# Kernel optimization log

Hardware: AMD Instinct MI355X
Metric: run time of the kernel (lower is better)

Reference implementation:

```python
import math
import jax, jax.numpy as jnp
import numpy as np

NQ = 4   # n_qubits
NL = 2   # n_layers
H = 16   # num_heads


def _apply_gate(state, gate, q, batched):
    """Apply a 1-qubit gate on wire q to batched state [N, 2**NQ]."""
    n = state.shape[0]
    left, right = 2 ** q, 2 ** (NQ - 1 - q)
    s = state.reshape(n, left, 2, right)
    eq = 'nab,nlbr->nlar' if batched else 'ab,nlbr->nlar'
    return jnp.einsum(eq, gate, s).reshape(n, 2 ** NQ)


def _rot(phi, theta, omega):
    """PennyLane Rot(phi, theta, omega) = RZ(omega) RY(theta) RZ(phi), 2x2 unitary."""
    c = jnp.cos(theta / 2).astype(jnp.complex64)
    s = jnp.sin(theta / 2).astype(jnp.complex64)
    ep = jnp.exp(-0.5j * (phi + omega).astype(jnp.complex64))
    em = jnp.exp(0.5j * (phi - omega).astype(jnp.complex64))
    m00 = ep * c
    m01 = -em * s
    m10 = jnp.conj(em) * s
    m11 = jnp.conj(ep) * c
    return jnp.stack([jnp.stack([m00, m01]), jnp.stack([m10, m11])])


def _cnot01(state):
    """CNOT with control wire 0, target wire 1 on [N, 16]."""
    n = state.shape[0]
    s = state.reshape(n, 2, 2, 2 ** (NQ - 2))
    s = jnp.stack([s[:, 0], s[:, 1, ::-1]], axis=1)
    return s.reshape(n, 2 ** NQ)


def _quantum_block(inputs, params):
    """Analytic state-vector simulation of the PennyLane circuit.

    inputs: [N, NQ] rotation angles (AngleEmbedding, default RX).
    params: [NL, NQ, 3] Rot parameters.
    Returns [N, NQ] Pauli-Z expectation values.
    """
    n = inputs.shape[0]
    state = jnp.zeros((n, 2 ** NQ), jnp.complex64).at[:, 0].set(1.0)
    # AngleEmbedding: RX(inputs[:, q]) on wire q
    for q in range(NQ):
        a = inputs[:, q] * 0.5
        c = jnp.cos(a).astype(jnp.complex64)
        s = (-1j) * jnp.sin(a).astype(jnp.complex64)
        gate = jnp.stack([jnp.stack([c, s], -1), jnp.stack([s, c], -1)], -2)  # [N,2,2]
        state = _apply_gate(state, gate, q, batched=True)
    # Variational layers
    for l in range(NL):
        for q in range(NQ):
            g = _rot(params[l, q, 0], params[l, q, 1], params[l, q, 2])
            state = _apply_gate(state, g, q, batched=False)
        state = _cnot01(state)
    probs = (jnp.abs(state) ** 2).reshape(n, 2, 2, 2, 2)
    z = jnp.array([1.0, -1.0], probs.dtype)
    letters = 'abcd'
    evs = [jnp.einsum(f'nabcd,{letters[i]}->n', probs, z) for i in range(NQ)]
    return jnp.stack(evs, axis=-1)


def reference(x, params, w_q, w_k, w_v, w_o):
    B, S, E = x.shape
    dk = E // H

    def proj(w):
        return (x @ w.T).reshape(B, S, H, dk).transpose(0, 2, 1, 3)  # [B,H,S,dk]

    q, k, v = proj(w_q), proj(w_k), proj(w_v)

    def inject(t):
        ang = t[..., :NQ].reshape(-1, NQ)
        ev = _quantum_block(ang, params).reshape(B, H, S, NQ).astype(t.dtype)
        return t.at[..., :NQ].set(ev)

    q, k, v = inject(q), inject(k), inject(v)
    scores = jnp.einsum('bhqd,bhkd->bhqk', q, k) / math.sqrt(dk)
    attn = jax.nn.softmax(scores, axis=-1)
    out = jnp.einsum('bhqk,bhkd->bhqd', attn, v)
    out = out.transpose(0, 2, 1, 3).reshape(B, S, E)
    return out @ w_o.T


def setup_inputs() -> dict:
    key = jax.random.key(0)
    ks = jax.random.split(key, 6)
    B, S, E = 2, 2048, 1024
    scale = 1.0 / math.sqrt(E)
    return {
        'x': jax.random.normal(ks[0], (B, S, E), jnp.float32),
        'params': jax.random.normal(ks[1], (NL, NQ, 3), jnp.float32),
        'w_q': jax.random.normal(ks[2], (E, E), jnp.float32) * scale,
        'w_k': jax.random.normal(ks[3], (E, E), jnp.float32) * scale,
        'w_v': jax.random.normal(ks[4], (E, E), jnp.float32) * scale,
        'w_o': jax.random.normal(ks[5], (E, E), jnp.float32) * scale,
    }
```

## Files before the change

### kernel.cpp

```cpp
#include <hip/hip_runtime.h>
#include <math.h>

#define BATCH 2
#define S_LEN 2048
#define E_DIM 1024
#define NHEAD 16
#define DK 64
#define NROWS (BATCH * S_LEN)

#define SM_A    0.18033688011f
#define SM_INVA 5.5451774444795623f
#define SM_B   -4.32808512267f

typedef _Float16 f16x8 __attribute__((ext_vector_type(8)));
typedef _Float16 f16x4 __attribute__((ext_vector_type(4)));
typedef float    f32x4 __attribute__((ext_vector_type(4)));

__device__ __forceinline__ void glds16(_Float16* lds, const _Float16* g) {
    __builtin_amdgcn_global_load_lds(
        (const __attribute__((address_space(1))) unsigned int*)g,
        (__attribute__((address_space(3))) unsigned int*)lds,
        16, 0, 0);
}

__global__ __launch_bounds__(256) void conv_all(
    const float* __restrict__ x,  const float* __restrict__ wq,
    const float* __restrict__ wk, const float* __restrict__ wv,
    const float* __restrict__ wo,
    _Float16* __restrict__ xh,  _Float16* __restrict__ wqh,
    _Float16* __restrict__ wkh, _Float16* __restrict__ wvh,
    _Float16* __restrict__ woh) {
    const int id = blockIdx.x;
    const float* src; _Float16* dst; int lid;
    if (id < 4096)      { src = x;  dst = xh;  lid = id; }
    else if (id < 5120) { src = wq; dst = wqh; lid = id - 4096; }
    else if (id < 6144) { src = wk; dst = wkh; lid = id - 5120; }
    else if (id < 7168) { src = wv; dst = wvh; lid = id - 6144; }
    else                { src = wo; dst = woh; lid = id - 7168; }
    const int i = lid * 256 + threadIdx.x;
    float4 v = ((const float4*)src)[i];
    f16x4 h;
    h[0] = (_Float16)v.x; h[1] = (_Float16)v.y;
    h[2] = (_Float16)v.z; h[3] = (_Float16)v.w;
    ((f16x4*)dst)[i] = h;
}

__device__ __forceinline__ void gemm_body(const _Float16* __restrict__ X,
                                          const _Float16* __restrict__ W,
                                          void* __restrict__ dstv, int mode,
                                          float oscale, _Float16* smem) {
    const int tid  = threadIdx.x;
    const int lane = tid & 63;
    const int w    = tid >> 6;
    const int wy = w >> 1, wx = w & 1;
    const int l15 = lane & 15, quad = lane >> 4;
    const int sw  = l15 & 7;
    const int m0 = blockIdx.y * 128, c0 = blockIdx.x * 128;

    const int lrow = lane >> 3;
    const int gcol = ((lane & 7) ^ lrow) * 8;
    const _Float16* xg = X + (size_t)(m0 + w * 32 + lrow) * E_DIM + gcol;
    const _Float16* wg = W + (size_t)(c0 + w * 32 + lrow) * E_DIM + gcol;
    const int woff = (w * 32) * 64;

    f32x4 acc[4][4];
#pragma unroll
    for (int i = 0; i < 4; ++i)
#pragma unroll
        for (int j = 0; j < 4; ++j) acc[i][j] = 0.f;

#pragma unroll
    for (int c = 0; c < 4; ++c) {
        glds16(smem + woff + c * 512,        xg + (size_t)c * 8 * E_DIM);
        glds16(smem + 8192 + woff + c * 512, wg + (size_t)c * 8 * E_DIM);
    }
    __syncthreads();

    for (int t = 0; t < E_DIM / 64; ++t) {
        const int buf = t & 1;
        _Float16* Xs = smem + buf * 16384;
        _Float16* Ws = Xs + 8192;
        if (t < E_DIM / 64 - 1) {
            _Float16* Xn = smem + (buf ^ 1) * 16384;
            const int k0 = (t + 1) * 64;
#pragma unroll
            for (int c = 0; c < 4; ++c) {
                glds16(Xn + woff + c * 512,        xg + (size_t)c * 8 * E_DIM + k0);
                glds16(Xn + 8192 + woff + c * 512, wg + (size_t)c * 8 * E_DIM + k0);
            }
        }

#pragma unroll
        for (int ks = 0; ks < 2; ++ks) {
            f16x8 af[4], bf[4];
#pragma unroll
            for (int i = 0; i < 4; ++i) {
                const int pc = ((ks * 4 + quad) ^ sw) * 8;
                af[i] = *(const f16x8*)&Xs[(wy * 64 + i * 16 + l15) * 64 + pc];
                bf[i] = *(const f16x8*)&Ws[(wx * 64 + i * 16 + l15) * 64 + pc];
            }
#pragma unroll
            for (int i = 0; i < 4; ++i)
#pragma unroll
                for (int j = 0; j < 4; ++j)
                    acc[i][j] = __builtin_amdgcn_mfma_f32_16x16x32_f16(af[i], bf[j], acc[i][j], 0, 0, 0);
        }
        __syncthreads();
    }

    if (mode == 2) {
        _Float16* Ct = smem;
#pragma unroll
        for (int i = 0; i < 4; ++i)
#pragma unroll
            for (int j = 0; j < 4; ++j) {
                const int col  = wx * 64 + j * 16 + l15;
                const int rowb = wy * 64 + i * 16 + quad * 4;
                f16x4 pk;
#pragma unroll
                for (int r = 0; r < 4; ++r) pk[r] = (_Float16)(acc[i][j][r] * oscale);
                *(f16x4*)&Ct[col * 136 + rowb] = pk;
            }
        __syncthreads();
        const int b  = m0 >> 11;
        const int s0 = m0 & 2047;
#pragma unroll
        for (int it = 0; it < 8; ++it) {
            const int c   = it * 256 + tid;
            const int col = c >> 4;
            const int rc  = c & 15;
            f16x8 v = *(const f16x8*)&Ct[col * 136 + rc * 8];
            const int e = c0 + col, h = e >> 6, d = e & 63;
            *(f16x8*)((_Float16*)dstv + ((size_t)((b * NHEAD + h) * DK + d)) * S_LEN + s0 + rc * 8) = v;
        }
        return;
    }

#pragma unroll
    for (int i = 0; i < 4; ++i)
#pragma unroll
        for (int j = 0; j < 4; ++j)
#pragma unroll
            for (int r = 0; r < 4; ++r) {
                const int row = m0 + wy * 64 + i * 16 + quad * 4 + r;
                const int col = c0 + wx * 64 + j * 16 + l15;
                const int b = row >> 11, s = row & 2047;
                const int h = col >> 6,  d = col & 63;
                ((_Float16*)dstv)[(((size_t)(b * NHEAD + h) * S_LEN + s) * DK) + d] =
                    (_Float16)(acc[i][j][r] * oscale);
            }
}

__global__ __launch_bounds__(256, 2) void gemm_qkv(
    const _Float16* __restrict__ X,
    const _Float16* __restrict__ WQ, const _Float16* __restrict__ WK,
    const _Float16* __restrict__ WV,
    _Float16* __restrict__ Qh, _Float16* __restrict__ Kh,
    _Float16* __restrict__ VTh) {
    __shared__ __align__(16) _Float16 smem[2 * 16384];
    const int z = blockIdx.z;
    const _Float16* W = (z == 0) ? WQ : (z == 1) ? WK : WV;
    void* dst = (z == 0) ? (void*)Qh : (z == 1) ? (void*)Kh : (void*)VTh;
    const float osc = (z == 1) ? SM_A : 1.0f;
    gemm_body(X, W, dst, (z == 2) ? 2 : 1, osc, smem);
}

__global__ __launch_bounds__(256, 3) void gemm_out2(const _Float16* __restrict__ X,
                                                    const _Float16* __restrict__ W,
                                                    float* __restrict__ dst) {
    __shared__ __align__(16) _Float16 smem[2 * 12288];

    const int tid  = threadIdx.x;
    const int lane = tid & 63;
    const int w    = tid >> 6;
    const int wy = w >> 1, wx = w & 1;
    const int l15 = lane & 15, quad = lane >> 4;
    const int sw  = l15 & 7;
    const int m0 = blockIdx.y * 128, c0 = blockIdx.x * 64;

    const int lrow = lane >> 3;
    const int gcol = ((lane & 7) ^ lrow) * 8;
    const _Float16* xg = X + (size_t)(m0 + w * 32 + lrow) * E_DIM + gcol;
    const _Float16* wg = W + (size_t)(c0 + w * 16 + lrow) * E_DIM + gcol;
    const int xoff = (w * 32) * 64;
    const int woff = (w * 16) * 64;

    f32x4 acc[4][2];
#pragma unroll
    for (int i = 0; i < 4; ++i)
#pragma unroll
        for (int j = 0; j < 2; ++j) acc[i][j] = 0.f;

#pragma unroll
    for (int c = 0; c < 4; ++c)
        glds16(smem + xoff + c * 512, xg + (size_t)c * 8 * E_DIM);
#pragma unroll
    for (int c = 0; c < 2; ++c)
        glds16(smem + 8192 + woff + c * 512, wg + (size_t)c * 8 * E_DIM);
    __syncthreads();

    for (int t = 0; t < E_DIM / 64; ++t) {
        const int buf = t & 1;
        _Float16* Xs = smem + buf * 12288;
        _Float16* Ws = Xs + 8192;
        if (t < E_DIM / 64 - 1) {
            _Float16* Xn = smem + (buf ^ 1) * 12288;
            const int k0 = (t + 1) * 64;
#pragma unroll
            for (int c = 0; c < 4; ++c)
                glds16(Xn + xoff + c * 512, xg + (size_t)c * 8 * E_DIM + k0);
#pragma unroll
            for (int c = 0; c < 2; ++c)
                glds16(Xn + 8192 + woff + c * 512, wg + (size_t)c * 8 * E_DIM + k0);
        }

#pragma unroll
        for (int ks = 0; ks < 2; ++ks) {
            f16x8 af[4], bf[2];
#pragma unroll
            for (int i = 0; i < 4; ++i) {
                const int pc = ((ks * 4 + quad) ^ sw) * 8;
                af[i] = *(const f16x8*)&Xs[(wy * 64 + i * 16 + l15) * 64 + pc];
            }
#pragma unroll
            for (int j = 0; j < 2; ++j) {
                const int pc = ((ks * 4 + quad) ^ sw) * 8;
                bf[j] = *(const f16x8*)&Ws[(wx * 32 + j * 16 + l15) * 64 + pc];
            }
#pragma unroll
            for (int i = 0; i < 4; ++i)
#pragma unroll
                for (int j = 0; j < 2; ++j)
                    acc[i][j] = __builtin_amdgcn_mfma_f32_16x16x32_f16(af[i], bf[j], acc[i][j], 0, 0, 0);
        }
        __syncthreads();
    }

#pragma unroll
    for (int i = 0; i < 4; ++i)
#pragma unroll
        for (int j = 0; j < 2; ++j)
#pragma unroll
            for (int r = 0; r < 4; ++r) {
                const int row = m0 + wy * 64 + i * 16 + quad * 4 + r;
                const int col = c0 + wx * 32 + j * 16 + l15;
                dst[(size_t)row * E_DIM + col] = acc[i][j][r];
            }
}

__device__ __forceinline__ void apply_gate(float ar[16], float ai[16], int stride,
                                           float g00r, float g00i, float g01r, float g01i,
                                           float g10r, float g10i, float g11r, float g11i) {
#pragma unroll
    for (int i0 = 0; i0 < 16; ++i0) {
        if (i0 & stride) continue;
        const int i1 = i0 + stride;
        const float s0r = ar[i0], s0i = ai[i0];
        const float s1r = ar[i1], s1i = ai[i1];
        ar[i0] = g00r * s0r - g00i * s0i + g01r * s1r - g01i * s1i;
        ai[i0] = g00r * s0i + g00i * s0r + g01r * s1i + g01i * s1r;
        ar[i1] = g10r * s0r - g10i * s0i + g11r * s1r - g11i * s1i;
        ai[i1] = g10r * s0i + g10i * s0r + g11r * s1i + g11i * s1r;
    }
}

__global__ __launch_bounds__(256) void quantum_inject(_Float16* __restrict__ Q,
                                                      _Float16* __restrict__ K,
                                                      _Float16* __restrict__ VT,
                                                      const float* __restrict__ params) {
    const int id = blockIdx.x * 256 + threadIdx.x;
    const int which = id >> 16;
    const int rem = id & 65535;

    float angv[4];
    _Float16* qkbase = nullptr;
    _Float16* vbase  = nullptr;
    if (which == 2) {
        const int bh = rem >> 11, s = rem & 2047;
        vbase = VT + ((size_t)bh * DK) * S_LEN + s;
#pragma unroll
        for (int d = 0; d < 4; ++d) angv[d] = (float)vbase[(size_t)d * S_LEN];
    } else {
        qkbase = (which == 0 ? Q : K) + (size_t)rem * DK;
        const f16x4 a4 = *(const f16x4*)qkbase;
        const float asc = (which == 1) ? SM_INVA : 1.0f;
#pragma unroll
        for (int d = 0; d < 4; ++d) angv[d] = (float)a4[d] * asc;
    }

    float ar[16], ai[16];
#pragma unroll
    for (int i = 0; i < 16; ++i) { ar[i] = 0.f; ai[i] = 0.f; }
    ar[0] = 1.f;

#pragma unroll
    for (int q = 0; q < 4; ++q) {
        float sh, ch;
        sincosf(0.5f * angv[q], &sh, &ch);
        apply_gate(ar, ai, 8 >> q, ch, 0.f, 0.f, -sh, 0.f, -sh, ch, 0.f);
    }

#pragma unroll
    for (int l = 0; l < 2; ++l) {
#pragma unroll
        for (int q = 0; q < 4; ++q) {
            const float* pp = params + (l * 4 + q) * 3;
            const float phi = pp[0], th = pp[1], om = pp[2];
            float st, ct, sa, ca, sb, cb;
            sincosf(0.5f * th, &st, &ct);
            sincosf(0.5f * (phi + om), &sa, &ca);
            sincosf(0.5f * (phi - om), &sb, &cb);
            apply_gate(ar, ai, 8 >> q,
                       ct * ca, -ct * sa,
                       -st * cb, -st * sb,
                       st * cb, -st * sb,
                       ct * ca, ct * sa);
        }
#pragma unroll
        for (int r = 0; r < 4; ++r) {
            float tr = ar[8 + r], ti = ai[8 + r];
            ar[8 + r] = ar[12 + r]; ai[8 + r] = ai[12 + r];
            ar[12 + r] = tr;        ai[12 + r] = ti;
        }
    }

    float ev[4] = {0.f, 0.f, 0.f, 0.f};
#pragma unroll
    for (int i = 0; i < 16; ++i) {
        const float p = ar[i] * ar[i] + ai[i] * ai[i];
        ev[0] += (i & 8) ? -p : p;
        ev[1] += (i & 4) ? -p : p;
        ev[2] += (i & 2) ? -p : p;
        ev[3] += (i & 1) ? -p : p;
    }
    if (which == 2) {
#pragma unroll
        for (int d = 0; d < 4; ++d) vbase[(size_t)d * S_LEN] = (_Float16)ev[d];
    } else {
        const float osc = (which == 1) ? SM_A : 1.0f;
        f16x4 o;
#pragma unroll
        for (int d = 0; d < 4; ++d) o[d] = (_Float16)(ev[d] * osc);
        *(f16x4*)qkbase = o;
    }
}

__global__ __launch_bounds__(256, 3) void attn10(const _Float16* __restrict__ Q,
                                                 const _Float16* __restrict__ K,
                                                 const _Float16* __restrict__ VT,
                                                 _Float16* __restrict__ ctx) {
    __shared__ __align__(16) _Float16 KVs[3][2][64 * 64];

    const int tid = threadIdx.x, lane = tid & 63, w = tid >> 6;
    const int l15 = lane & 15, quad = lane >> 4;
    const int sw  = l15 & 7;
    const int bh = blockIdx.y;
    const int qbase = blockIdx.x * 128 + w * 32;

    const _Float16* Qb = Q  + (size_t)bh * S_LEN * DK;
    const _Float16* Kb = K  + (size_t)bh * S_LEN * DK;
    const _Float16* Vb = VT + (size_t)bh * DK * S_LEN;

    const int lrow = lane >> 3;
    const int gcol = ((lane & 7) ^ lrow) * 8;
    const int sr0  = 32 * (w >> 1) + 8 * (lrow >> 2) + 4 * (w & 1) + (lrow & 3);
    const _Float16* kg = Kb + (size_t)sr0 * DK + gcol;
    const _Float16* vg = Vb + (size_t)(w * 16 + lrow) * S_LEN + gcol;

    auto stage = [&](int u, int bidx) {
        const int kt = u * 64;
        _Float16* kb = &KVs[bidx][0][(w * 16) * 64];
        _Float16* vb = &KVs[bidx][1][(w * 16) * 64];
        glds16(kb,       kg + (size_t)kt * DK);
        glds16(kb + 512, kg + (size_t)(kt + 16) * DK);
        glds16(vb,       vg + (size_t)kt);
        glds16(vb + 512, vg + (size_t)8 * S_LEN + kt);
    };

    f16x8 bf[2][2];
#pragma unroll
    for (int qn = 0; qn < 2; ++qn)
#pragma unroll
        for (int ks = 0; ks < 2; ++ks)
            bf[qn][ks] = *(const f16x8*)(Qb + (size_t)(qbase + qn * 16 + l15) * DK + ks * 32 + quad * 8);

    f32x4 oacc[4][2];
#pragma unroll
    for (int dt = 0; dt < 4; ++dt)
#pragma unroll
        for (int qn = 0; qn < 2; ++qn) oacc[dt][qn] = 0.f;
    float lpart[2] = {0.f, 0.f};

    stage(0, 0);
    stage(1, 1);
    asm volatile("s_waitcnt vmcnt(4)" ::: "memory");
    __builtin_amdgcn_s_barrier();

    int buf = 0, nbuf = 2;
    for (int t = 0; t < S_LEN / 64; ++t) {
        if (t < S_LEN / 64 - 2) stage(t + 2, nbuf);

        f16x8 af[4][2], vt[4][2];
#pragma unroll
        for (int kc = 0; kc < 4; ++kc)
#pragma unroll
            for (int ks = 0; ks < 2; ++ks)
                af[kc][ks] = *(const f16x8*)&KVs[buf][0][(kc * 16 + l15) * 64 + ((ks * 4 + quad) ^ sw) * 8];
#pragma unroll
        for (int dt = 0; dt < 4; ++dt)
#pragma unroll
            for (int kh = 0; kh < 2; ++kh)
                vt[dt][kh] = *(const f16x8*)&KVs[buf][1][(dt * 16 + l15) * 64 + ((kh * 4 + quad) ^ sw) * 8];

        f16x4 pk4s[4][2];
#pragma unroll
        for (int kc = 0; kc < 4; ++kc)
#pragma unroll
            for (int qn = 0; qn < 2; ++qn) {
                f32x4 st = SM_B;
                st = __builtin_amdgcn_mfma_f32_16x16x32_f16(af[kc][0], bf[qn][0], st, 0, 0, 0);
                st = __builtin_amdgcn_mfma_f32_16x16x32_f16(af[kc][1], bf[qn][1], st, 0, 0, 0);
                float ps = 0.f;
                f16x4 pk;
#pragma unroll
                for (int r = 0; r < 4; ++r) {
                    const float p = __builtin_amdgcn_exp2f(st[r]);
                    ps += p;
                    pk[r] = (_Float16)p;
                }
                lpart[qn] += ps;
                pk4s[kc][qn] = pk;
            }

#pragma unroll
        for (int dt = 0; dt < 4; ++dt)
#pragma unroll
            for (int qn = 0; qn < 2; ++qn)
#pragma unroll
                for (int kh = 0; kh < 2; ++kh) {
                    const f16x8 pb = __builtin_shufflevector(
                        pk4s[2 * kh][qn], pk4s[2 * kh + 1][qn],
                        0, 1, 2, 3, 4, 5, 6, 7);
                    oacc[dt][qn] = __builtin_amdgcn_mfma_f32_16x16x32_f16(
                        vt[dt][kh], pb, oacc[dt][qn], 0, 0, 0);
                }

        if (t < S_LEN / 64 - 2) {
            asm volatile("s_waitcnt vmcnt(4)" ::: "memory");
        } else if (t == S_LEN / 64 - 2) {
            asm volatile("s_waitcnt vmcnt(0)" ::: "memory");
        }
        __builtin_amdgcn_s_barrier();

        buf  = (buf == 2)  ? 0 : buf + 1;
        nbuf = (nbuf == 2) ? 0 : nbuf + 1;
    }

    float inv[2];
#pragma unroll
    for (int qn = 0; qn < 2; ++qn) {
        float l = lpart[qn];
        l += __shfl_xor(l, 16);
        l += __shfl_xor(l, 32);
        inv[qn] = 1.f / l;
    }

    _Float16* ep = &KVs[0][0][0] + w * (32 * 72);
#pragma unroll
    for (int dt = 0; dt < 4; ++dt)
#pragma unroll
        for (int qn = 0; qn < 2; ++qn) {
            f16x4 ov;
#pragma unroll
            for (int r = 0; r < 4; ++r) ov[r] = (_Float16)(oacc[dt][qn][r] * inv[qn]);
            *(f16x4*)&ep[(qn * 16 + l15) * 72 + dt * 16 + quad * 4] = ov;
        }

    const int b = bh >> 4, h = bh & 15;
#pragma unroll
    for (int i = 0; i < 4; ++i) {
        const int c = i * 64 + lane;
        const int row = c >> 3, c8 = c & 7;
        f16x8 v = *(const f16x8*)&ep[row * 72 + c8 * 8];
        *(f16x8*)(ctx + (size_t)(b * S_LEN + qbase + row) * E_DIM + h * DK + c8 * 8) = v;
    }
}

extern "C" void kernel_launch(void* const* d_in, const int* in_sizes, int n_in,
                              void* d_out, int out_size, void* d_ws, size_t ws_size,
                              hipStream_t stream) {
    const float* x      = (const float*)d_in[0];
    const float* params = (const float*)d_in[1];
    const float* w_q    = (const float*)d_in[2];
    const float* w_k    = (const float*)d_in[3];
    const float* w_v    = (const float*)d_in[4];
    const float* w_o    = (const float*)d_in[5];
    float* out = (float*)d_out;

    const size_t TENS = (size_t)NROWS * E_DIM;
    const size_t WEL  = (size_t)E_DIM * E_DIM;
    _Float16* xh  = (_Float16*)d_ws;
    _Float16* wqh = xh  + TENS;
    _Float16* wkh = wqh + WEL;
    _Float16* wvh = wkh + WEL;
    _Float16* woh = wvh + WEL;
    _Float16* Qh  = woh + WEL;
    _Float16* Kh  = Qh  + TENS;
    _Float16* VTh = Kh  + TENS;
    _Float16* CTXh= VTh + TENS;

    dim3 blk(256);

    conv_all<<<dim3(8192), blk, 0, stream>>>(x, w_q, w_k, w_v, w_o,
                                             xh, wqh, wkh, wvh, woh);

    gemm_qkv<<<dim3(E_DIM / 128, NROWS / 128, 3), blk, 0, stream>>>(
        xh, wqh, wkh, wvh, Qh, Kh, VTh);

    quantum_inject<<<dim3(768), blk, 0, stream>>>(Qh, Kh, VTh, params);

    attn10<<<dim3(S_LEN / 128, BATCH * NHEAD), blk, 0, stream>>>(Qh, Kh, VTh, CTXh);

    gemm_out2<<<dim3(E_DIM / 64, NROWS / 128), blk, 0, stream>>>(CTXh, woh, out);
}
```

Before: 187.9 us.

## Halve QKV GEMM k-tile to 32 to cut LDS and raise occupancy

The QKV projection GEMM now stages 32-wide k-slices instead of 64, which halves its shared-memory footprint and lets the launch bound ask for four blocks per CU instead of two. The swizzle and load mapping are adjusted to the narrower rows. The V-transpose epilogue is split into two half-width phases so it fits in the smaller buffer. In exchange there are twice as many k-iterations and barriers, and fewer MFMAs per synchronization.

```diff
diff --git a/kernel.cpp b/kernel.cpp
--- a/kernel.cpp
+++ b/kernel.cpp
@@ -45,23 +45,23 @@
     ((f16x4*)dst)[i] = h;
 }
 
-__device__ __forceinline__ void gemm_body(const _Float16* __restrict__ X,
-                                          const _Float16* __restrict__ W,
-                                          void* __restrict__ dstv, int mode,
-                                          float oscale, _Float16* smem) {
+__device__ __forceinline__ void gemm_body32(const _Float16* __restrict__ X,
+                                            const _Float16* __restrict__ W,
+                                            void* __restrict__ dstv, int mode,
+                                            float oscale, _Float16* smem) {
     const int tid  = threadIdx.x;
     const int lane = tid & 63;
     const int w    = tid >> 6;
     const int wy = w >> 1, wx = w & 1;
     const int l15 = lane & 15, quad = lane >> 4;
-    const int sw  = l15 & 7;
+    const int sw3 = l15 & 3;
     const int m0 = blockIdx.y * 128, c0 = blockIdx.x * 128;
 
-    const int lrow = lane >> 3;
-    const int gcol = ((lane & 7) ^ lrow) * 8;
+    const int lrow = lane >> 2;
+    const int gcol = ((lane & 3) ^ (lrow & 3)) * 8;
     const _Float16* xg = X + (size_t)(m0 + w * 32 + lrow) * E_DIM + gcol;
     const _Float16* wg = W + (size_t)(c0 + w * 32 + lrow) * E_DIM + gcol;
-    const int woff = (w * 32) * 64;
+    const int woff = (w * 32) * 32;
 
     f32x4 acc[4][4];
 #pragma unroll
@@ -69,69 +69,72 @@
 #pragma unroll
         for (int j = 0; j < 4; ++j) acc[i][j] = 0.f;
 
-#pragma unroll
-    for (int c = 0; c < 4; ++c) {
-        glds16(smem + woff + c * 512,        xg + (size_t)c * 8 * E_DIM);
-        glds16(smem + 8192 + woff + c * 512, wg + (size_t)c * 8 * E_DIM);
-    }
+    glds16(smem + woff,              xg);
+    glds16(smem + woff + 512,        xg + (size_t)16 * E_DIM);
+    glds16(smem + 4096 + woff,       wg);
+    glds16(smem + 4096 + woff + 512, wg + (size_t)16 * E_DIM);
     __syncthreads();
 
-    for (int t = 0; t < E_DIM / 64; ++t) {
+    for (int t = 0; t < E_DIM / 32; ++t) {
         const int buf = t & 1;
-        _Float16* Xs = smem + buf * 16384;
-        _Float16* Ws = Xs + 8192;
-        if (t < E_DIM / 64 - 1) {
-            _Float16* Xn = smem + (buf ^ 1) * 16384;
-            const int k0 = (t + 1) * 64;
-#pragma unroll
-            for (int c = 0; c < 4; ++c) {
-                glds16(Xn + woff + c * 512,        xg + (size_t)c * 8 * E_DIM + k0);
-                glds16(Xn + 8192 + woff + c * 512, wg + (size_t)c * 8 * E_DIM + k0);
-            }
-        }
-
-#pragma unroll
-        for (int ks = 0; ks < 2; ++ks) {
-            f16x8 af[4], bf[4];
-#pragma unroll
-            for (int i = 0; i < 4; ++i) {
-                const int pc = ((ks * 4 + quad) ^ sw) * 8;
-                af[i] = *(const f16x8*)&Xs[(wy * 64 + i * 16 + l15) * 64 + pc];
-                bf[i] = *(const f16x8*)&Ws[(wx * 64 + i * 16 + l15) * 64 + pc];
-            }
-#pragma unroll
-            for (int i = 0; i < 4; ++i)
-#pragma unroll
-                for (int j = 0; j < 4; ++j)
-                    acc[i][j] = __builtin_amdgcn_mfma_f32_16x16x32_f16(af[i], bf[j], acc[i][j], 0, 0, 0);
-        }
+        _Float16* Xs = smem + buf * 8192;
+        _Float16* Ws = Xs + 4096;
+        if (t < E_DIM / 32 - 1) {
+            _Float16* Xn = smem + (buf ^ 1) * 8192;
+            const int k0 = (t + 1) * 32;
+            glds16(Xn + woff,              xg + k0);
+            glds16(Xn + woff + 512,        xg + (size_t)16 * E_DIM + k0);
+            glds16(Xn + 4096 + woff,       wg + k0);
+            glds16(Xn + 4096 + woff + 512, wg + (size_t)16 * E_DIM + k0);
+        }
+
+        f16x8 af[4], bf[4];
+        const int pc = (quad ^ sw3) * 8;
+#pragma unroll
+        for (int i = 0; i < 4; ++i)
+            af[i] = *(const f16x8*)&Xs[(wy * 64 + i * 16 + l15) * 32 + pc];
+#pragma unroll
+        for (int j = 0; j < 4; ++j)
+            bf[j] = *(const f16x8*)&Ws[(wx * 64 + j * 16 + l15) * 32 + pc];
+#pragma unroll
+        for (int i = 0; i < 4; ++i)
+#pragma unroll
+            for (int j = 0; j < 4; ++j)
+                acc[i][j] = __builtin_amdgcn_mfma_f32_16x16x32_f16(af[i], bf[j], acc[i][j], 0, 0, 0);
+
         __syncthreads();
     }
 
     if (mode == 2) {
         _Float16* Ct = smem;
-#pragma unroll
-        for (int i = 0; i < 4; ++i)
-#pragma unroll
-            for (int j = 0; j < 4; ++j) {
-                const int col  = wx * 64 + j * 16 + l15;
-                const int rowb = wy * 64 + i * 16 + quad * 4;
-                f16x4 pk;
-#pragma unroll
-                for (int r = 0; r < 4; ++r) pk[r] = (_Float16)(acc[i][j][r] * oscale);
-                *(f16x4*)&Ct[col * 136 + rowb] = pk;
-            }
-        __syncthreads();
         const int b  = m0 >> 11;
         const int s0 = m0 & 2047;
 #pragma unroll
-        for (int it = 0; it < 8; ++it) {
-            const int c   = it * 256 + tid;
-            const int col = c >> 4;
-            const int rc  = c & 15;
-            f16x8 v = *(const f16x8*)&Ct[col * 136 + rc * 8];
-            const int e = c0 + col, h = e >> 6, d = e & 63;
-            *(f16x8*)((_Float16*)dstv + ((size_t)((b * NHEAD + h) * DK + d)) * S_LEN + s0 + rc * 8) = v;
+        for (int hph = 0; hph < 2; ++hph) {
+            if (wx == hph) {
+#pragma unroll
+                for (int i = 0; i < 4; ++i)
+#pragma unroll
+                    for (int j = 0; j < 4; ++j) {
+                        const int col_l = j * 16 + l15;
+                        const int rowb  = wy * 64 + i * 16 + quad * 4;
+                        f16x4 pk;
+#pragma unroll
+                        for (int r = 0; r < 4; ++r) pk[r] = (_Float16)(acc[i][j][r] * oscale);
+                        *(f16x4*)&Ct[col_l * 136 + rowb] = pk;
+                    }
+            }
+            __syncthreads();
+#pragma unroll
+            for (int it = 0; it < 4; ++it) {
+                const int c     = it * 256 + tid;
+                const int col_l = c >> 4;
+                const int rc    = c & 15;
+                f16x8 v = *(const f16x8*)&Ct[col_l * 136 + rc * 8];
+                const int e = c0 + hph * 64 + col_l, h = e >> 6, d = e & 63;
+                *(f16x8*)((_Float16*)dstv + ((size_t)((b * NHEAD + h) * DK + d)) * S_LEN + s0 + rc * 8) = v;
+            }
+            __syncthreads();
         }
         return;
     }
@@ -151,18 +154,18 @@
             }
 }
 
-__global__ __launch_bounds__(256, 2) void gemm_qkv(
+__global__ __launch_bounds__(256, 4) void gemm_qkv(
     const _Float16* __restrict__ X,
     const _Float16* __restrict__ WQ, const _Float16* __restrict__ WK,
     const _Float16* __restrict__ WV,
     _Float16* __restrict__ Qh, _Float16* __restrict__ Kh,
     _Float16* __restrict__ VTh) {
-    __shared__ __align__(16) _Float16 smem[2 * 16384];
+    __shared__ __align__(16) _Float16 smem[2 * 8192];
     const int z = blockIdx.z;
     const _Float16* W = (z == 0) ? WQ : (z == 1) ? WK : WV;
     void* dst = (z == 0) ? (void*)Qh : (z == 1) ? (void*)Kh : (void*)VTh;
     const float osc = (z == 1) ? SM_A : 1.0f;
-    gemm_body(X, W, dst, (z == 2) ? 2 : 1, osc, smem);
+    gemm_body32(X, W, dst, (z == 2) ? 2 : 1, osc, smem);
 }
 
 __global__ __launch_bounds__(256, 3) void gemm_out2(const _Float16* __restrict__ X,
```

Measured after the change: 185.3 us. Within noise of the previous version (-1.4%).
